# Kernel optimization log

Hardware: AMD Instinct MI355X
Metric: run time of the kernel (lower is better)

The kernel has to match this reference:

```python
import jax, jax.numpy as jnp
import numpy as np

C = 1024
H = C // 64          # 16 heads
CH = 64              # head dim
NUM_BUCKETS = 32
MAX_DISTANCE = 64
REL_SCALE = float(np.sqrt(CH))  # (channels//num_heads)**0.5 = 8
EPS = 1e-5


def group_norm(x, gamma, beta, groups):
    # x: [B, C, T]
    B, Cc, T = x.shape
    xg = x.reshape(B, groups, -1)
    m = xg.mean(-1, keepdims=True)
    v = xg.var(-1, keepdims=True)
    xn = ((xg - m) * jax.lax.rsqrt(v + EPS)).reshape(B, Cc, T)
    return xn * gamma[None, :, None] + beta[None, :, None]


def conv1d(x, w, b, pad):
    # x: [B, Cin, T], w: [Cout, Cin, K]
    y = jax.lax.conv_general_dilated(x, w, (1,), [(pad, pad)],
                                     dimension_numbers=('NCH', 'OIH', 'NCH'))
    return y + b[None, :, None]


def rel_pos_bias(T, emb):
    # lucidrains RelativePositionBias, non-causal; emb: [num_buckets, H]
    pos = jnp.arange(T)
    n = pos[:, None] - pos[None, :]          # n = -(k - q) = q - k
    half = NUM_BUCKETS // 2                  # 16
    ret = (n < 0).astype(jnp.int32) * half
    n = jnp.abs(n)
    max_exact = half // 2                    # 8
    is_small = n < max_exact
    nf = jnp.maximum(n, 1).astype(jnp.float32)
    val_large = max_exact + (jnp.log(nf / max_exact)
                             / np.log(MAX_DISTANCE / max_exact)
                             * (half - max_exact)).astype(jnp.int32)
    val_large = jnp.minimum(val_large, half - 1)
    bucket = ret + jnp.where(is_small, n, val_large)  # [T, T]
    return emb[bucket].transpose(2, 0, 1)             # [H, T, T]


def setup_inputs() -> dict:
    key = jax.random.key(0)
    ks = jax.random.split(key, 20)
    B, T = 8, 1024
    s = 0.02
    return {
        'x': jax.random.normal(ks[0], (B, C, T), jnp.float32),
        # ResBlock in_layers
        'rb_gn1_g': jnp.ones((C,), jnp.float32),
        'rb_gn1_b': jnp.zeros((C,), jnp.float32),
        'rb_conv1_w': jax.random.normal(ks[1], (C, C, 3), jnp.float32) * s,
        'rb_conv1_b': jnp.zeros((C,), jnp.float32),
        # ResBlock out_layers (zero-init in original; randomized for testing)
        'rb_gn2_g': jnp.ones((C,), jnp.float32),
        'rb_gn2_b': jnp.zeros((C,), jnp.float32),
        'rb_conv2_w': jax.random.normal(ks[2], (C, C, 3), jnp.float32) * s,
        'rb_conv2_b': jnp.zeros((C,), jnp.float32),
        # outer GroupNorm(8, C)
        'norm_g': jnp.ones((C,), jnp.float32),
        'norm_b': jnp.zeros((C,), jnp.float32),
        # AttentionBlock
        'attn_gn_g': jnp.ones((C,), jnp.float32),
        'attn_gn_b': jnp.zeros((C,), jnp.float32),
        'qkv_w': jax.random.normal(ks[3], (3 * C, C, 1), jnp.float32) * s,
        'qkv_b': jnp.zeros((3 * C,), jnp.float32),
        'proj_w': jax.random.normal(ks[4], (C, C, 1), jnp.float32) * s,
        'proj_b': jnp.zeros((C,), jnp.float32),
        'rel_emb': jax.random.normal(ks[5], (NUM_BUCKETS, H), jnp.float32) * s,
    }


def reference(x, rb_gn1_g, rb_gn1_b, rb_conv1_w, rb_conv1_b,
              rb_gn2_g, rb_gn2_b, rb_conv2_w, rb_conv2_b,
              norm_g, norm_b, attn_gn_g, attn_gn_b,
              qkv_w, qkv_b, proj_w, proj_b, rel_emb):
    B, Cc, T = x.shape
    # ResBlock: GN32 -> SiLU -> conv3 -> GN32 -> SiLU -> (dropout=0) -> conv3, + skip
    h = jax.nn.silu(group_norm(x, rb_gn1_g, rb_gn1_b, 32))
    h = conv1d(h, rb_conv1_w, rb_conv1_b, 1)
    h = jax.nn.silu(group_norm(h, rb_gn2_g, rb_gn2_b, 32))
    h = conv1d(h, rb_conv2_w, rb_conv2_b, 1)
    h = x + h
    # outer GroupNorm(8)
    h = group_norm(h, norm_g, norm_b, 8)
    # AttentionBlock with relative position bias
    xin = h
    qkv = conv1d(group_norm(h, attn_gn_g, attn_gn_b, 32), qkv_w, qkv_b, 0)
    # channel layout after reshape(bs*H, 3*ch, T): [H, 3, ch]
    qkv = qkv.reshape(B, H, 3, CH, T)
    q, k, v = qkv[:, :, 0], qkv[:, :, 1], qkv[:, :, 2]
    scale = CH ** -0.25
    w = jnp.einsum('bhct,bhcs->bhts', q * scale, k * scale)
    bias = rel_pos_bias(T, rel_emb) * REL_SCALE       # [H, T, T]
    w = jax.nn.softmax((w + bias[None]).astype(jnp.float32), axis=-1).astype(w.dtype)
    a = jnp.einsum('bhts,bhcs->bhct', w, v).reshape(B, Cc, T)
    return xin + conv1d(a, proj_w, proj_b, 0)
```

## Files before the change

kernel.cpp:

```cpp
#include <hip/hip_runtime.h>

typedef __attribute__((ext_vector_type(4))) float f32x4;
typedef __attribute__((ext_vector_type(8))) __bf16 bf16x8;
typedef __attribute__((ext_vector_type(4))) unsigned short us4;
typedef __attribute__((ext_vector_type(8))) unsigned short us8;

#define DEVI static __device__ __forceinline__

DEVI unsigned short f2bf(float f){
  union { float f; unsigned u; } x; x.f = f;
  unsigned r = x.u + 0x7fffu + ((x.u >> 16) & 1u);
  return (unsigned short)(r >> 16);
}
DEVI float bf2f(unsigned short h){
  union { unsigned u; float f; } x; x.u = ((unsigned)h) << 16;
  return x.f;
}

typedef __attribute__((address_space(1))) unsigned int gu32;
typedef __attribute__((address_space(3))) unsigned int lu32;
DEVI void gll16(const void* g, void* l){
  __builtin_amdgcn_global_load_lds((gu32*)g, (lu32*)l, 16, 0, 0);
}

DEVI f32x4 mfma16(bf16x8 a, bf16x8 b, f32x4 c){
  return __builtin_amdgcn_mfma_f32_16x16x32_bf16(a, b, c, 0, 0, 0);
}

DEVI float wredsum(float v){
  #pragma unroll
  for (int m = 1; m < 64; m <<= 1) v += __shfl_xor(v, m);
  return v;
}

__global__ __launch_bounds__(256) void conv_w_prep(const float* __restrict__ w,
                                                   unsigned short* __restrict__ wp){
  int idx = blockIdx.x * 256 + threadIdx.x;
  const float* p = w + (size_t)idx * 3;
  wp[idx]           = f2bf(p[0]);
  wp[1048576 + idx] = f2bf(p[1]);
  wp[2097152 + idx] = f2bf(p[2]);
}

__global__ __launch_bounds__(256) void cast_f2b(const float* __restrict__ in,
                                                unsigned short* __restrict__ out, int n4){
  int idx = blockIdx.x * 256 + threadIdx.x;
  if (idx < n4){
    f32x4 v = *(const f32x4*)&in[(size_t)idx * 4];
    us4 o;
    #pragma unroll
    for (int j = 0; j < 4; j++) o[j] = f2bf(v[j]);
    *(us4*)&out[(size_t)idx * 4] = o;
  }
}

__global__ __launch_bounds__(256) void btab_k(const float* __restrict__ emb,
                                              float* __restrict__ btab){
  int idx = blockIdx.x * 256 + threadIdx.x;
  if (idx >= 2047 * 16) return;
  int d = idx >> 4, h = idx & 15;
  int n0 = d - 1023;
  int ret = (n0 < 0) ? 16 : 0;
  int n = (n0 < 0) ? -n0 : n0;
  int bucket;
  if (n < 8) bucket = ret + n;
  else {
    float ratio = logf((float)n * 0.125f) / 2.0794415416798357f;
    int vl = 8 + (int)(ratio * 8.0f);
    bucket = ret + (vl < 15 ? vl : 15);
  }
  btab[h * 2048 + d] = emb[bucket * 16 + h] * 11.541560327111707f;
}

__global__ __launch_bounds__(256) void zero_pads(unsigned short* __restrict__ h1p,
                                                 unsigned short* __restrict__ g2p){
  int idx = blockIdx.x * 256 + threadIdx.x;
  int b = idx >> 11, rr = (idx >> 10) & 1, c = idx & 1023;
  size_t off = ((size_t)b * 1026 + (rr ? 1025 : 0)) * 1024 + c;
  h1p[off] = 0; g2p[off] = 0;
}

__global__ __launch_bounds__(256) void gn_stats_f32(const float* __restrict__ in,
                                                    float2* __restrict__ st){
  const int g = blockIdx.x; const int tid = threadIdx.x;
  const float* p = in + (size_t)g * 32768;
  float s = 0.f, s2 = 0.f;
  for (int i = tid * 4; i < 32768; i += 1024){
    f32x4 v = *(const f32x4*)&p[i];
    #pragma unroll
    for (int j = 0; j < 4; j++){ s += v[j]; s2 += v[j] * v[j]; }
  }
  s = wredsum(s); s2 = wredsum(s2);
  __shared__ float rs[4], rs2[4];
  if ((tid & 63) == 0){ rs[tid >> 6] = s; rs2[tid >> 6] = s2; }
  __syncthreads();
  if (tid == 0){
    float S = rs[0] + rs[1] + rs[2] + rs[3];
    float S2 = rs2[0] + rs2[1] + rs2[2] + rs2[3];
    float m = S * (1.f / 32768.f);
    float var = S2 * (1.f / 32768.f) - m * m;
    st[g] = make_float2(m, rsqrtf(var + 1e-5f));
  }
}

__global__ __launch_bounds__(256) void gn_stats_bf16(const unsigned short* __restrict__ in,
                                                     float2* __restrict__ st){
  const int g = blockIdx.x; const int tid = threadIdx.x;
  const unsigned short* p = in + (size_t)g * 32768;
  float s = 0.f, s2 = 0.f;
  for (int i = tid * 8; i < 32768; i += 2048){
    us8 v = *(const us8*)&p[i];
    #pragma unroll
    for (int j = 0; j < 8; j++){ float f = bf2f(v[j]); s += f; s2 += f * f; }
  }
  s = wredsum(s); s2 = wredsum(s2);
  __shared__ float rs[4], rs2[4];
  if ((tid & 63) == 0){ rs[tid >> 6] = s; rs2[tid >> 6] = s2; }
  __syncthreads();
  if (tid == 0){
    float S = rs[0] + rs[1] + rs[2] + rs[3];
    float S2 = rs2[0] + rs2[1] + rs2[2] + rs2[3];
    float m = S * (1.f / 32768.f);
    float var = S2 * (1.f / 32768.f) - m * m;
    st[g] = make_float2(m, rsqrtf(var + 1e-5f));
  }
}

template<int SILU, int INBF16, int OUTPAD>
__global__ __launch_bounds__(256) void gn_apply_tr(
    const void* __restrict__ inp, const float2* __restrict__ st,
    const float* __restrict__ gma, const float* __restrict__ bta,
    unsigned short* __restrict__ out)
{
  const int gid = blockIdx.x;
  const int tc = gid & 15, g = (gid >> 4) & 31, b = gid >> 9;
  const int tid = threadIdx.x;
  const int t0 = tc * 64;
  __shared__ __align__(16) unsigned short tr[64 * 40];
  float2 s = st[b * 32 + g];
  int c = tid >> 3, t8 = (tid & 7) * 8;
  int ch = g * 32 + c;
  float sc = gma[ch] * s.y;
  float sh = bta[ch] - s.x * sc;
  float vv[8];
  if (INBF16){
    const unsigned short* p = (const unsigned short*)inp + ((size_t)b * 1024 + ch) * 1024 + t0 + t8;
    us8 v = *(const us8*)p;
    #pragma unroll
    for (int j = 0; j < 8; j++) vv[j] = bf2f(v[j]);
  } else {
    const float* p = (const float*)inp + ((size_t)b * 1024 + ch) * 1024 + t0 + t8;
    f32x4 v0 = *(const f32x4*)p; f32x4 v1 = *(const f32x4*)(p + 4);
    #pragma unroll
    for (int j = 0; j < 4; j++){ vv[j] = v0[j]; vv[4 + j] = v1[j]; }
  }
  #pragma unroll
  for (int j = 0; j < 8; j++){
    float v = vv[j] * sc + sh;
    if (SILU) v = v / (1.f + __expf(-v));
    tr[(t8 + j) * 40 + c] = f2bf(v);
  }
  __syncthreads();
  int t = tid >> 2, c8 = (tid & 3) * 8;
  us8 d = *(const us8*)&tr[t * 40 + c8];
  size_t row = OUTPAD ? ((size_t)b * 1026 + 1 + t0 + t) : ((size_t)b * 1024 + t0 + t);
  *(us8*)&out[row * 1024 + g * 32 + c8] = d;
}

__global__ __launch_bounds__(256) void gn2_partial(const unsigned short* __restrict__ c1,
                                                   float2* __restrict__ part){
  const int tid = threadIdx.x;
  const int ck = blockIdx.x & 31, b = blockIdx.x >> 5;
  const unsigned short* p = c1 + ((size_t)b * 1024 + ck * 32) * 1024 + tid * 4;
  float s = 0.f, s2 = 0.f;
  for (int r = 0; r < 32; r++){
    us4 v = *(const us4*)&p[(size_t)r * 1024];
    #pragma unroll
    for (int j = 0; j < 4; j++){ float f = bf2f(v[j]); s += f; s2 += f * f; }
  }
  __shared__ float ls[256], ls2[256];
  ls[tid] = s; ls2[tid] = s2;
  __syncthreads();
  if (tid < 32){
    float S = 0.f, S2 = 0.f;
    #pragma unroll
    for (int k = 0; k < 8; k++){ S += ls[tid * 8 + k]; S2 += ls2[tid * 8 + k]; }
    part[((size_t)b * 32 + ck) * 32 + tid] = make_float2(S, S2);
  }
}

template<int SILU>
__global__ __launch_bounds__(256) void gn2_apply(const unsigned short* __restrict__ c1,
    const float2* __restrict__ part, const float* __restrict__ gma, const float* __restrict__ bta,
    unsigned short* __restrict__ outp)
{
  const int tid = threadIdx.x;
  const int ck = blockIdx.x & 31, b = blockIdx.x >> 5;
  __shared__ float2 st[32];
  if (tid < 32){
    float S = 0.f, S2 = 0.f;
    for (int k = 0; k < 32; k++){ float2 pp = part[((size_t)b * 32 + k) * 32 + tid]; S += pp.x; S2 += pp.y; }
    float m = S * (1.f / 32768.f);
    float var = S2 * (1.f / 32768.f) - m * m;
    st[tid] = make_float2(m, rsqrtf(var + 1e-5f));
  }
  __syncthreads();
  float2 s = st[tid >> 3];
  float sc[4], sh[4];
  #pragma unroll
  for (int j = 0; j < 4; j++){ int ch = tid * 4 + j; sc[j] = gma[ch] * s.y; sh[j] = bta[ch] - s.x * sc[j]; }
  const unsigned short* p = c1 + ((size_t)b * 1024 + ck * 32) * 1024 + tid * 4;
  unsigned short* q = outp + ((size_t)b * 1026 + 1 + ck * 32) * 1024 + tid * 4;
  for (int r = 0; r < 32; r++){
    us4 v = *(const us4*)&p[(size_t)r * 1024];
    us4 o;
    #pragma unroll
    for (int j = 0; j < 4; j++){
      float f = bf2f(v[j]) * sc[j] + sh[j];
      if (SILU) f = f / (1.f + __expf(-f));
      o[j] = f2bf(f);
    }
    *(us4*)&q[(size_t)r * 1024] = o;
  }
}

__global__ __launch_bounds__(256) void gn8_partial(const float* __restrict__ r,
                                                   float2* __restrict__ part){
  const int gid = blockIdx.x; const int tid = threadIdx.x;
  const int sub = gid & 15, g = (gid >> 4) & 7, b = gid >> 7;
  const float* p = r + ((size_t)(b * 8 + g)) * 131072 + sub * 8192;
  float s = 0.f, s2 = 0.f;
  for (int i = tid * 8; i < 8192; i += 2048){
    f32x4 v0 = *(const f32x4*)&p[i], v1 = *(const f32x4*)&p[i + 4];
    #pragma unroll
    for (int j = 0; j < 4; j++){ s += v0[j] + v1[j]; s2 += v0[j] * v0[j] + v1[j] * v1[j]; }
  }
  s = wredsum(s); s2 = wredsum(s2);
  __shared__ float rs[4], rs2[4];
  if ((tid & 63) == 0){ rs[tid >> 6] = s; rs2[tid >> 6] = s2; }
  __syncthreads();
  if (tid == 0) part[gid] = make_float2(rs[0] + rs[1] + rs[2] + rs[3],
                                        rs2[0] + rs2[1] + rs2[2] + rs2[3]);
}

__global__ __launch_bounds__(256) void gn8_apply(const float* __restrict__ r,
    const float2* __restrict__ part, const float* __restrict__ gma, const float* __restrict__ bta,
    unsigned short* __restrict__ xin){
  const int gid = blockIdx.x; const int tid = threadIdx.x;
  const int sub = gid & 15, g = (gid >> 4) & 7, b = gid >> 7;
  __shared__ float2 stt;
  if (tid == 0){
    float S = 0.f, S2 = 0.f;
    #pragma unroll
    for (int k = 0; k < 16; k++){ float2 pp = part[(gid & ~15) + k]; S += pp.x; S2 += pp.y; }
    float m = S * (1.f / 131072.f);
    float var = S2 * (1.f / 131072.f) - m * m;
    stt = make_float2(m, rsqrtf(var + 1e-5f));
  }
  __syncthreads();
  float2 s = stt;
  const float* pr = r + ((size_t)(b * 8 + g)) * 131072 + sub * 8192;
  unsigned short* px = xin + ((size_t)(b * 8 + g)) * 131072 + sub * 8192;
  for (int i = tid * 8; i < 8192; i += 2048){
    int c = g * 128 + sub * 8 + (i >> 10);
    float sc = gma[c] * s.y, sh = bta[c] - s.x * sc;
    f32x4 v0 = *(const f32x4*)&pr[i], v1 = *(const f32x4*)&pr[i + 4];
    us8 o;
    #pragma unroll
    for (int j = 0; j < 4; j++){ o[j] = f2bf(v0[j] * sc + sh); o[4 + j] = f2bf(v1[j] * sc + sh); }
    *(us8*)&px[i] = o;
  }
}

template<int KK, int EPI>
__global__ __launch_bounds__(256, 2) void gemm_k(
    const unsigned short* __restrict__ inT,
    const unsigned short* __restrict__ W,
    const float* __restrict__ bias,
    void* __restrict__ outp,
    void* __restrict__ resp,
    int OC, int NT)
{
  __shared__ __align__(16) unsigned short Alds[128 * 64];
  __shared__ __align__(16) unsigned short Blds[128 * 64];
  const int tid = threadIdx.x;
  const int lane = tid & 63;
  const int w = tid >> 6;
  const int wn = w >> 1, wo = w & 1;
  const int nt = blockIdx.x % NT;
  const int ot = blockIdx.x / NT;
  const int b = nt >> 3;
  const int t0 = (nt & 7) * 128;
  const int ob = ot * 128;
  const int rowbase = (KK == 3) ? (b * 1026 + t0) : (b * 1024 + t0);

  f32x4 acc[4][4];
  #pragma unroll
  for (int m = 0; m < 4; m++)
    #pragma unroll
    for (int n = 0; n < 4; n++) acc[m][n] = 0.f;

  const int lrow = lane >> 3;
  const int lblk = lane & 7;

  for (int kk = 0; kk < KK; ++kk){
    const unsigned short* Ab = inT + (size_t)(rowbase + kk) * 1024;
    const unsigned short* Bb = W + ((size_t)kk * OC + ob) * 1024;
    for (int i0 = 0; i0 < 1024; i0 += 64){
      #pragma unroll
      for (int j = 0; j < 4; ++j){
        int chunk = w * 4 + j;
        int row = chunk * 8 + lrow;
        int gcol = (lblk ^ (row & 7)) * 8;
        gll16(Ab + (size_t)row * 1024 + i0 + gcol, &Alds[chunk * 512]);
        gll16(Bb + (size_t)row * 1024 + i0 + gcol, &Blds[chunk * 512]);
      }
      __syncthreads();
      bf16x8 af[2][4], bfv[2][4];
      #pragma unroll
      for (int m = 0; m < 4; m++){
        int row = wn * 64 + m * 16 + (lane & 15);
        #pragma unroll
        for (int k2 = 0; k2 < 2; k2++){
          int blk = ((lane >> 4) + k2 * 4) ^ (row & 7);
          af[k2][m] = *(const bf16x8*)&Alds[row * 64 + blk * 8];
        }
      }
      #pragma unroll
      for (int n = 0; n < 4; n++){
        int row = wo * 64 + n * 16 + (lane & 15);
        #pragma unroll
        for (int k2 = 0; k2 < 2; k2++){
          int blk = ((lane >> 4) + k2 * 4) ^ (row & 7);
          bfv[k2][n] = *(const bf16x8*)&Blds[row * 64 + blk * 8];
        }
      }
      #pragma unroll
      for (int k2 = 0; k2 < 2; k2++)
        #pragma unroll
        for (int m = 0; m < 4; m++)
          #pragma unroll
          for (int n = 0; n < 4; n++)
            acc[m][n] = mfma16(af[k2][m], bfv[k2][n], acc[m][n]);
      __syncthreads();
    }
  }

  if (EPI == 0){
    unsigned short* out = (unsigned short*)outp;
    #pragma unroll
    for (int m = 0; m < 4; m++){
      int tl = t0 + wn * 64 + m * 16 + ((lane >> 4) * 4);
      #pragma unroll
      for (int n = 0; n < 4; n++){
        int o = ob + wo * 64 + n * 16 + (lane & 15);
        float bz = bias[o];
        size_t base = ((size_t)b * 1024 + tl) * OC + o;
        #pragma unroll
        for (int r = 0; r < 4; r++)
          out[base + (size_t)r * OC] = f2bf(acc[m][n][r] + bz);
      }
    }
  } else if (EPI == 3){
    unsigned short* qkT = (unsigned short*)outp;
    unsigned short* vT  = (unsigned short*)resp;
    #pragma unroll
    for (int m = 0; m < 4; m++){
      int tl = t0 + wn * 64 + m * 16 + ((lane >> 4) * 4);
      #pragma unroll
      for (int n = 0; n < 4; n++){
        int o0 = ob + wo * 64 + n * 16;
        int h = o0 / 192;
        int rem0 = o0 - h * 192;
        int o = o0 + (lane & 15);
        float bz = bias[o];
        if (rem0 < 128){
          size_t base = ((size_t)b * 1024 + tl) * 2048 + h * 128 + rem0 + (lane & 15);
          #pragma unroll
          for (int r = 0; r < 4; r++)
            qkT[base + (size_t)r * 2048] = f2bf(acc[m][n][r] + bz);
        } else {
          int c = rem0 - 128 + (lane & 15);
          size_t base = (((size_t)(b * 16 + h)) * 64 + c) * 1024 + tl;
          us4 o4;
          #pragma unroll
          for (int r = 0; r < 4; r++) o4[r] = f2bf(acc[m][n][r] + bz);
          *(us4*)&vT[base] = o4;
        }
      }
    }
  } else {
    float* out = (float*)outp;
    #pragma unroll
    for (int m = 0; m < 4; m++){
      int tl = t0 + wn * 64 + m * 16 + ((lane >> 4) * 4);
      #pragma unroll
      for (int n = 0; n < 4; n++){
        int o = ob + wo * 64 + n * 16 + (lane & 15);
        float bz = bias[o];
        size_t base = ((size_t)b * 1024 + o) * 1024 + tl;
        f32x4 v;
        if (EPI == 1){
          const float* xr = (const float*)resp;
          v = *(const f32x4*)&xr[base];
        } else {
          const unsigned short* xr = (const unsigned short*)resp;
          us4 xv = *(const us4*)&xr[base];
          v[0] = bf2f(xv[0]); v[1] = bf2f(xv[1]); v[2] = bf2f(xv[2]); v[3] = bf2f(xv[3]);
        }
        #pragma unroll
        for (int r = 0; r < 4; r++) v[r] += acc[m][n][r] + bz;
        *(f32x4*)&out[base] = v;
      }
    }
  }
}

__global__ __launch_bounds__(256, 2) void attn_k3(
    const unsigned short* __restrict__ qkT,
    const unsigned short* __restrict__ vT,
    const float* __restrict__ btab,
    unsigned short* __restrict__ aT)
{
  __shared__ __align__(16) unsigned short Kb[2][64 * 64];
  __shared__ __align__(16) unsigned short Vb[2][64 * 64];
  __shared__ __align__(16) unsigned short Pb[4][32 * 64];
  const int tid = threadIdx.x, lane = tid & 63, w = tid >> 6;
  const int d0 = blockIdx.x;
  const int xcd = d0 & 7, slot = d0 >> 3;
  const int bh = xcd * 16 + (slot >> 3);
  const int qt = slot & 7;
  const int h = bh & 15, b = bh >> 4;
  const int q0 = qt * 128 + w * 32;
  const unsigned short* qk = qkT + (size_t)b * 1024 * 2048 + h * 128;
  const unsigned short* vh = vT + ((size_t)(b * 16 + h)) * 64 * 1024;
  const int lc = lane & 15, lg = lane >> 4;

  bf16x8 qf[2][2];
  #pragma unroll
  for (int m = 0; m < 2; m++){
    const unsigned short* qrow = qk + (size_t)(q0 + m * 16 + lc) * 2048;
    #pragma unroll
    for (int k2 = 0; k2 < 2; k2++)
      qf[m][k2] = *(const bf16x8*)&qrow[k2 * 32 + lg * 8];
  }
  float m_run[2], l_run[2];
  f32x4 oacc[2][4];
  m_run[0] = m_run[1] = -1e30f; l_run[0] = l_run[1] = 0.f;
  #pragma unroll
  for (int m = 0; m < 2; m++)
    #pragma unroll
    for (int cb = 0; cb < 4; cb++) oacc[m][cb] = 0.f;

  const int lr = lane >> 3, lb = lane & 7;
  const float* bth = btab + h * 2048 + 1023;
  const float qs = 0.18033688011112042f;

  #pragma unroll
  for (int j = 0; j < 2; j++){
    int chunk = w * 2 + j;
    int row = chunk * 8 + lr;
    int gcol = (lb ^ (row & 7)) * 8;
    gll16(qk + 64 + (size_t)row * 2048 + gcol, &Kb[0][chunk * 512]);
    gll16(vh + (size_t)row * 1024 + gcol, &Vb[0][chunk * 512]);
  }
  __syncthreads();

  for (int t = 0; t < 16; ++t){
    const int cur = t & 1;
    const int st0 = t * 64;
    if (t < 15){
      int nst = st0 + 64;
      #pragma unroll
      for (int j = 0; j < 2; j++){
        int chunk = w * 2 + j;
        int row = chunk * 8 + lr;
        int gcol = (lb ^ (row & 7)) * 8;
        gll16(qk + 64 + (size_t)(nst + row) * 2048 + gcol, &Kb[cur ^ 1][chunk * 512]);
        gll16(vh + (size_t)row * 1024 + nst + gcol, &Vb[cur ^ 1][chunk * 512]);
      }
    }
    f32x4 sfr[2][4];
    #pragma unroll
    for (int m = 0; m < 2; m++)
      #pragma unroll
      for (int sub = 0; sub < 4; sub++) sfr[m][sub] = 0.f;
    #pragma unroll
    for (int sub = 0; sub < 4; sub++){
      int row = sub * 16 + lc;
      #pragma unroll
      for (int k2 = 0; k2 < 2; k2++){
        int blk = (lg + k2 * 4) ^ (row & 7);
        bf16x8 bk = *(const bf16x8*)&Kb[cur][row * 64 + blk * 8];
        sfr[0][sub] = mfma16(bk, qf[0][k2], sfr[0][sub]);
        sfr[1][sub] = mfma16(bk, qf[1][k2], sfr[1][sub]);
      }
    }
    float corr[2];
    #pragma unroll
    for (int m = 0; m < 2; m++){
      const float* btq = bth + (q0 + m * 16 + lc) - st0;
      #pragma unroll
      for (int sub = 0; sub < 4; sub++){
        int sl = sub * 16 + lg * 4;
        #pragma unroll
        for (int r = 0; r < 4; r++)
          sfr[m][sub][r] = sfr[m][sub][r] * qs + btq[-(sl + r)];
      }
      float v = fmaxf(fmaxf(sfr[m][0][0], sfr[m][0][1]), fmaxf(sfr[m][0][2], sfr[m][0][3]));
      #pragma unroll
      for (int sub = 1; sub < 4; sub++)
        v = fmaxf(v, fmaxf(fmaxf(sfr[m][sub][0], sfr[m][sub][1]),
                           fmaxf(sfr[m][sub][2], sfr[m][sub][3])));
      v = fmaxf(v, __shfl_xor(v, 16));
      v = fmaxf(v, __shfl_xor(v, 32));
      float mn = fmaxf(m_run[m], v);
      corr[m] = exp2f(m_run[m] - mn);
      m_run[m] = mn;
      float ssum = 0.f;
      #pragma unroll
      for (int sub = 0; sub < 4; sub++)
        #pragma unroll
        for (int r = 0; r < 4; r++){
          float e = exp2f(sfr[m][sub][r] - mn);
          sfr[m][sub][r] = e;
          ssum += e;
        }
      ssum += __shfl_xor(ssum, 16);
      ssum += __shfl_xor(ssum, 32);
      l_run[m] = l_run[m] * corr[m] + ssum;
    }
    #pragma unroll
    for (int m = 0; m < 2; m++)
      #pragma unroll
      for (int r = 0; r < 4; r++){
        float co = __shfl(corr[m], lg * 4 + r);
        #pragma unroll
        for (int cb = 0; cb < 4; cb++) oacc[m][cb][r] *= co;
      }
    unsigned short* P = &Pb[w][0];
    #pragma unroll
    for (int m = 0; m < 2; m++){
      int qrow = m * 16 + lc;
      int rsw = (qrow & 7) << 3;
      #pragma unroll
      for (int sub = 0; sub < 4; sub++){
        int col = sub * 16 + lg * 4;
        unsigned w0, w1;
        asm("v_cvt_pk_bf16_f32 %0, %1, %2" : "=v"(w0) : "v"(sfr[m][sub][0]), "v"(sfr[m][sub][1]));
        asm("v_cvt_pk_bf16_f32 %0, %1, %2" : "=v"(w1) : "v"(sfr[m][sub][2]), "v"(sfr[m][sub][3]));
        uint2 pk; pk.x = w0; pk.y = w1;
        *(uint2*)&P[qrow * 64 + (col ^ rsw)] = pk;
      }
    }
    #pragma unroll
    for (int k2 = 0; k2 < 2; k2++){
      bf16x8 pa[2];
      #pragma unroll
      for (int m = 0; m < 2; m++){
        int rowp = m * 16 + lc;
        int blkp = (lg + k2 * 4) ^ (rowp & 7);
        pa[m] = *(const bf16x8*)&P[rowp * 64 + blkp * 8];
      }
      #pragma unroll
      for (int cb = 0; cb < 4; cb++){
        int ch = cb * 16 + lc;
        int blkv = (lg + k2 * 4) ^ (ch & 7);
        bf16x8 bv = *(const bf16x8*)&Vb[cur][ch * 64 + blkv * 8];
        oacc[0][cb] = mfma16(pa[0], bv, oacc[0][cb]);
        oacc[1][cb] = mfma16(pa[1], bv, oacc[1][cb]);
      }
    }
    __syncthreads();
  }
  #pragma unroll
  for (int m = 0; m < 2; m++)
    #pragma unroll
    for (int r = 0; r < 4; r++){
      float li = 1.0f / __shfl(l_run[m], lg * 4 + r);
      int tq = q0 + m * 16 + lg * 4 + r;
      #pragma unroll
      for (int cb = 0; cb < 4; cb++){
        int ch = h * 64 + cb * 16 + lc;
        aT[((size_t)b * 1024 + tq) * 1024 + ch] = f2bf(oacc[m][cb][r] * li);
      }
    }
}

extern "C" void kernel_launch(void* const* d_in, const int* in_sizes, int n_in,
                              void* d_out, int out_size, void* d_ws, size_t ws_size,
                              hipStream_t stream)
{
  const float* x       = (const float*)d_in[0];
  const float* gn1_g   = (const float*)d_in[1];
  const float* gn1_b   = (const float*)d_in[2];
  const float* conv1_w = (const float*)d_in[3];
  const float* conv1_b = (const float*)d_in[4];
  const float* gn2_g   = (const float*)d_in[5];
  const float* gn2_b   = (const float*)d_in[6];
  const float* conv2_w = (const float*)d_in[7];
  const float* conv2_b = (const float*)d_in[8];
  const float* norm_g  = (const float*)d_in[9];
  const float* norm_b  = (const float*)d_in[10];
  const float* agn_g   = (const float*)d_in[11];
  const float* agn_b   = (const float*)d_in[12];
  const float* qkv_w   = (const float*)d_in[13];
  const float* qkv_b   = (const float*)d_in[14];
  const float* proj_w  = (const float*)d_in[15];
  const float* proj_b  = (const float*)d_in[16];
  const float* rel_emb = (const float*)d_in[17];

  if (ws_size < 139526144u) return;

  char* ws = (char*)d_ws;
  unsigned short* w1p   = (unsigned short*)(ws + 0);
  unsigned short* w2p   = (unsigned short*)(ws + 6291456);
  unsigned short* wqkv  = (unsigned short*)(ws + 12582912);
  unsigned short* wproj = (unsigned short*)(ws + 18874368);
  float* btab           = (float*)(ws + 20971520);
  float2* stats1        = (float2*)(ws + 21102592);
  float2* part2         = (float2*)(ws + 21104640);
  float2* stats32       = (float2*)(ws + 21170176);
  float2* part8         = (float2*)(ws + 21172224);
  unsigned short* h1p   = (unsigned short*)(ws + 22020096);
  unsigned short* c1    = (unsigned short*)(ws + 38830080);
  unsigned short* g2p   = (unsigned short*)(ws + 55607296);
  unsigned short* qkT   = h1p;
  unsigned short* vT    = (unsigned short*)(ws + 55574528);
  float* rbuf           = (float*)(ws + 72417280);
  unsigned short* attn_in = (unsigned short*)(ws + 72417280);
  unsigned short* xin   = (unsigned short*)(ws + 105971712);
  unsigned short* aT    = (unsigned short*)(ws + 122748928);

  conv_w_prep<<<4096, 256, 0, stream>>>(conv1_w, w1p);
  conv_w_prep<<<4096, 256, 0, stream>>>(conv2_w, w2p);
  cast_f2b<<<3072, 256, 0, stream>>>(qkv_w, wqkv, 3072 * 1024 / 4);
  cast_f2b<<<1024, 256, 0, stream>>>(proj_w, wproj, 1024 * 1024 / 4);
  btab_k<<<128, 256, 0, stream>>>(rel_emb, btab);
  zero_pads<<<64, 256, 0, stream>>>(h1p, g2p);

  gn_stats_f32<<<256, 256, 0, stream>>>(x, stats1);
  gn_apply_tr<1, 0, 1><<<4096, 256, 0, stream>>>(x, stats1, gn1_g, gn1_b, h1p);

  gemm_k<3, 0><<<512, 256, 0, stream>>>(h1p, w1p, conv1_b, c1, nullptr, 1024, 64);

  gn2_partial<<<256, 256, 0, stream>>>(c1, part2);
  gn2_apply<1><<<256, 256, 0, stream>>>(c1, part2, gn2_g, gn2_b, g2p);

  gemm_k<3, 1><<<512, 256, 0, stream>>>(g2p, w2p, conv2_b, rbuf, (void*)x, 1024, 64);

  gn8_partial<<<1024, 256, 0, stream>>>(rbuf, part8);
  gn8_apply<<<1024, 256, 0, stream>>>(rbuf, part8, norm_g, norm_b, xin);

  gn_stats_bf16<<<256, 256, 0, stream>>>(xin, stats32);
  gn_apply_tr<0, 1, 0><<<4096, 256, 0, stream>>>(xin, stats32, agn_g, agn_b, attn_in);

  gemm_k<1, 3><<<1536, 256, 0, stream>>>(attn_in, wqkv, qkv_b, qkT, vT, 3072, 64);

  attn_k3<<<1024, 256, 0, stream>>>(qkT, vT, btab, aT);

  gemm_k<1, 2><<<512, 256, 0, stream>>>(aT, wproj, proj_b, d_out, xin, 1024, 64);
}
```

Measured before the change: 400.8 us.

## Stage bias table in LDS, skip softmax rescale when max stable, set MFMA priority

The attention kernel now loads the per-head relative bias slice into shared memory once per block instead of reading it from global memory each tile. It adds a lazy-rescale path that, when the new tile max stays within a threshold of the running max, skips the correction exponentials and the output-accumulator rescaling. It also raises wave priority around the MFMA sections. This trades extra shared memory and a wave-uniform branch for fewer global loads and less VALU work; the lazy path can let exponentials exceed one by a bounded factor.

```diff
diff --git a/kernel.cpp b/kernel.cpp
--- a/kernel.cpp
+++ b/kernel.cpp
@@ -416,7 +416,7 @@
   }
 }
 
-__global__ __launch_bounds__(256, 2) void attn_k3(
+__global__ __launch_bounds__(256, 2) void attn_k4(
     const unsigned short* __restrict__ qkT,
     const unsigned short* __restrict__ vT,
     const float* __restrict__ btab,
@@ -425,17 +425,22 @@
   __shared__ __align__(16) unsigned short Kb[2][64 * 64];
   __shared__ __align__(16) unsigned short Vb[2][64 * 64];
   __shared__ __align__(16) unsigned short Pb[4][32 * 64];
+  __shared__ __align__(16) float blds[1152];
   const int tid = threadIdx.x, lane = tid & 63, w = tid >> 6;
   const int d0 = blockIdx.x;
   const int xcd = d0 & 7, slot = d0 >> 3;
   const int bh = xcd * 16 + (slot >> 3);
   const int qt = slot & 7;
   const int h = bh & 15, b = bh >> 4;
-  const int q0 = qt * 128 + w * 32;
+  const int q0b = qt * 128;
+  const int q0 = q0b + w * 32;
   const unsigned short* qk = qkT + (size_t)b * 1024 * 2048 + h * 128;
   const unsigned short* vh = vT + ((size_t)(b * 16 + h)) * 64 * 1024;
   const int lc = lane & 15, lg = lane >> 4;
 
+  for (int i = tid; i < 1151; i += 256)
+    blds[i] = btab[h * 2048 + q0b + i];
+
   bf16x8 qf[2][2];
   #pragma unroll
   for (int m = 0; m < 2; m++){
@@ -453,7 +458,6 @@
     for (int cb = 0; cb < 4; cb++) oacc[m][cb] = 0.f;
 
   const int lr = lane >> 3, lb = lane & 7;
-  const float* bth = btab + h * 2048 + 1023;
   const float qs = 0.18033688011112042f;
 
   #pragma unroll
@@ -485,6 +489,7 @@
     for (int m = 0; m < 2; m++)
       #pragma unroll
       for (int sub = 0; sub < 4; sub++) sfr[m][sub] = 0.f;
+    __builtin_amdgcn_s_setprio(1);
     #pragma unroll
     for (int sub = 0; sub < 4; sub++){
       int row = sub * 16 + lc;
@@ -496,48 +501,73 @@
         sfr[1][sub] = mfma16(bk, qf[1][k2], sfr[1][sub]);
       }
     }
-    float corr[2];
+    __builtin_amdgcn_s_setprio(0);
+    float pm2[2];
     #pragma unroll
     for (int m = 0; m < 2; m++){
-      const float* btq = bth + (q0 + m * 16 + lc) - st0;
+      const float* bp = &blds[(w * 32 + m * 16 + lc) + 960 - st0];
       #pragma unroll
       for (int sub = 0; sub < 4; sub++){
-        int sl = sub * 16 + lg * 4;
+        int off = 63 - sub * 16 - lg * 4;
         #pragma unroll
         for (int r = 0; r < 4; r++)
-          sfr[m][sub][r] = sfr[m][sub][r] * qs + btq[-(sl + r)];
-      }
-      float v = fmaxf(fmaxf(sfr[m][0][0], sfr[m][0][1]), fmaxf(sfr[m][0][2], sfr[m][0][3]));
-      #pragma unroll
-      for (int sub = 1; sub < 4; sub++)
-        v = fmaxf(v, fmaxf(fmaxf(sfr[m][sub][0], sfr[m][sub][1]),
-                           fmaxf(sfr[m][sub][2], sfr[m][sub][3])));
-      v = fmaxf(v, __shfl_xor(v, 16));
-      v = fmaxf(v, __shfl_xor(v, 32));
-      float mn = fmaxf(m_run[m], v);
-      corr[m] = exp2f(m_run[m] - mn);
-      m_run[m] = mn;
-      float ssum = 0.f;
-      #pragma unroll
-      for (int sub = 0; sub < 4; sub++)
+          sfr[m][sub][r] = sfr[m][sub][r] * qs + bp[off - r];
+      }
+      float x0 = fmaxf(fmaxf(sfr[m][0][0], sfr[m][0][1]), fmaxf(sfr[m][0][2], sfr[m][0][3]));
+      float x1 = fmaxf(fmaxf(sfr[m][1][0], sfr[m][1][1]), fmaxf(sfr[m][1][2], sfr[m][1][3]));
+      float x2 = fmaxf(fmaxf(sfr[m][2][0], sfr[m][2][1]), fmaxf(sfr[m][2][2], sfr[m][2][3]));
+      float x3 = fmaxf(fmaxf(sfr[m][3][0], sfr[m][3][1]), fmaxf(sfr[m][3][2], sfr[m][3][3]));
+      float pm = fmaxf(fmaxf(x0, x1), fmaxf(x2, x3));
+      pm = fmaxf(pm, __shfl_xor(pm, 16));
+      pm = fmaxf(pm, __shfl_xor(pm, 32));
+      pm2[m] = pm;
+    }
+    bool stable = (pm2[0] <= m_run[0] + 8.f) && (pm2[1] <= m_run[1] + 8.f);
+    if (__all(stable)){
+      #pragma unroll
+      for (int m = 0; m < 2; m++){
+        float ssum = 0.f;
+        #pragma unroll
+        for (int sub = 0; sub < 4; sub++)
+          #pragma unroll
+          for (int r = 0; r < 4; r++){
+            float e = exp2f(sfr[m][sub][r] - m_run[m]);
+            sfr[m][sub][r] = e;
+            ssum += e;
+          }
+        ssum += __shfl_xor(ssum, 16);
+        ssum += __shfl_xor(ssum, 32);
+        l_run[m] += ssum;
+      }
+    } else {
+      float corr[2];
+      #pragma unroll
+      for (int m = 0; m < 2; m++){
+        float mn = fmaxf(m_run[m], pm2[m]);
+        corr[m] = exp2f(m_run[m] - mn);
+        m_run[m] = mn;
+        float ssum = 0.f;
+        #pragma unroll
+        for (int sub = 0; sub < 4; sub++)
+          #pragma unroll
+          for (int r = 0; r < 4; r++){
+            float e = exp2f(sfr[m][sub][r] - mn);
+            sfr[m][sub][r] = e;
+            ssum += e;
+          }
+        ssum += __shfl_xor(ssum, 16);
+        ssum += __shfl_xor(ssum, 32);
+        l_run[m] = l_run[m] * corr[m] + ssum;
+      }
+      #pragma unroll
+      for (int m = 0; m < 2; m++)
         #pragma unroll
         for (int r = 0; r < 4; r++){
-          float e = exp2f(sfr[m][sub][r] - mn);
-          sfr[m][sub][r] = e;
-          ssum += e;
+          float co = __shfl(corr[m], lg * 4 + r);
+          #pragma unroll
+          for (int cb = 0; cb < 4; cb++) oacc[m][cb][r] *= co;
         }
-      ssum += __shfl_xor(ssum, 16);
-      ssum += __shfl_xor(ssum, 32);
-      l_run[m] = l_run[m] * corr[m] + ssum;
-    }
-    #pragma unroll
-    for (int m = 0; m < 2; m++)
-      #pragma unroll
-      for (int r = 0; r < 4; r++){
-        float co = __shfl(corr[m], lg * 4 + r);
-        #pragma unroll
-        for (int cb = 0; cb < 4; cb++) oacc[m][cb][r] *= co;
-      }
+    }
     unsigned short* P = &Pb[w][0];
     #pragma unroll
     for (int m = 0; m < 2; m++){
@@ -553,6 +583,7 @@
         *(uint2*)&P[qrow * 64 + (col ^ rsw)] = pk;
       }
     }
+    __builtin_amdgcn_s_setprio(1);
     #pragma unroll
     for (int k2 = 0; k2 < 2; k2++){
       bf16x8 pa[2];
@@ -571,6 +602,7 @@
         oacc[1][cb] = mfma16(pa[1], bv, oacc[1][cb]);
       }
     }
+    __builtin_amdgcn_s_setprio(0);
     __syncthreads();
   }
   #pragma unroll
@@ -657,7 +689,7 @@
 
   gemm_k<1, 3><<<1536, 256, 0, stream>>>(attn_in, wqkv, qkv_b, qkT, vT, 3072, 64);
 
-  attn_k3<<<1024, 256, 0, stream>>>(qkT, vT, btab, aT);
+  attn_k4<<<1024, 256, 0, stream>>>(qkT, vT, btab, aT);
 
   gemm_k<1, 2><<<512, 256, 0, stream>>>(aT, wproj, proj_b, d_out, xin, 1024, 64);
 }
```

After: 390.4 us. -2.6%, faster.
